# Performance work log

Hardware: AMD Instinct MI355X
Metric: run time of the kernel (lower is better)

Reference implementation:

```python
import jax, jax.numpy as jnp
import numpy as np

C = 0.01          # Poincare ball curvature 1/100
SQRT_C = 0.1
EPS = 1e-15
BALL_EPS = 4e-3   # geoopt float32 projx boundary epsilon


def _norm(x):
    return jnp.linalg.norm(x, axis=-1, keepdims=True)


def expmap0(u):
    n = jnp.maximum(_norm(u), EPS)
    return jnp.tanh(SQRT_C * n) * u / (SQRT_C * n)


def logmap0(x):
    n = jnp.maximum(_norm(x), EPS)
    t = jnp.clip(SQRT_C * n, -1.0 + 1e-7, 1.0 - 1e-7)
    return jnp.arctanh(t) * x / (SQRT_C * n)


def projx(x):
    maxnorm = (1.0 - BALL_EPS) / SQRT_C
    n = jnp.maximum(_norm(x), EPS)
    return jnp.where(n > maxnorm, x / n * maxnorm, x)


def mobius_matvec(M, x):
    xn = jnp.maximum(_norm(x), EPS)
    mx = x @ M.T
    mxn = jnp.maximum(_norm(mx), EPS)
    t = jnp.clip(SQRT_C * xn, -1.0 + 1e-7, 1.0 - 1e-7)
    res = jnp.tanh(mxn / xn * jnp.arctanh(t)) * mx / (mxn * SQRT_C)
    return jnp.where(jnp.all(mx == 0, axis=-1, keepdims=True), 0.0, res)


def mobius_add(x, y):
    x2 = jnp.sum(x * x, -1, keepdims=True)
    y2 = jnp.sum(y * y, -1, keepdims=True)
    xy = jnp.sum(x * y, -1, keepdims=True)
    num = (1 + 2 * C * xy + C * y2) * x + (1 - C * x2) * y
    den = 1 + 2 * C * xy + C * C * x2 * y2
    return num / jnp.maximum(den, EPS)


def hyp_linear(x, W, b):
    # eval mode: weight dropout is a no-op
    res = projx(mobius_matvec(W, x))
    hb = projx(expmap0(b.reshape(1, -1)))
    return projx(mobius_add(res, hb))


def setup_inputs() -> dict:
    key = jax.random.key(0)
    ks = jax.random.split(key, 10)
    B, S, N, H, HEADS, E = 2, 4, 10000, 64, 4, 160000
    G = B * S
    OC = H // HEADS
    # edges guaranteed to have no self-loops (module removes then re-adds them)
    src = jax.random.randint(ks[0], (G, E), 0, N)
    off = jax.random.randint(ks[1], (G, E), 1, N)
    dst = (src + off) % N
    edge_index = jnp.stack([src, dst], axis=1).astype(jnp.int32)  # [G,2,E]

    def glorot(k, shape, fan):
        a = np.sqrt(6.0 / fan)
        return jax.random.uniform(k, shape, minval=-a, maxval=a, dtype=jnp.float32)

    emb = jax.random.normal(ks[2], (N, H), dtype=jnp.float32)
    att_i = glorot(ks[3], (1, HEADS, OC), HEADS * OC + 1)
    att_j = glorot(ks[4], (1, HEADS, OC), HEADS * OC + 1)
    w1 = glorot(ks[5], (H, OC), H + OC)   # HypLinear(in=16, out=64): weight [out,in]
    b1 = jnp.zeros((H,), jnp.float32)
    w2 = glorot(ks[6], (H, H), H + H)
    b2 = jnp.zeros((H,), jnp.float32)
    history_graphs = jnp.zeros((B, S, N), jnp.float32)  # only shape is used
    return {"history_graphs": history_graphs, "edge_index": edge_index,
            "emb": emb, "att_i": att_i, "att_j": att_j,
            "w1": w1, "b1": b1, "w2": w2, "b2": b2}


def reference(history_graphs, edge_index, emb, att_i, att_j, w1, b1, w2, b2):
    B, S, N = history_graphs.shape
    G = edge_index.shape[0]
    H = emb.shape[1]
    heads = att_i.shape[1]
    oc = H // heads

    # node ids are arange(N) for every (b,s) -> identical features per graph
    x0 = projx(expmap0(emb))   # initHyperX, [N,H]
    xt = logmap0(x0)           # tangent features used by attention, [N,H]

    # add self loops (inputs contain none)
    loops = jnp.broadcast_to(jnp.arange(N, dtype=edge_index.dtype)[None, None, :], (G, 2, N))
    ei = jnp.concatenate([edge_index, loops], axis=-1)  # [G,2,E+N]

    def agg(e):
        src, dst = e[0], e[1]                       # targets (i), sources (j)
        x_i = xt[src].reshape(-1, heads, oc)        # [E2,h,oc]
        x_j = xt[dst].reshape(-1, heads, oc)
        alpha = jnp.sum(x_i * att_i, -1) + jnp.sum(x_j * att_j, -1)  # [E2,h]
        alpha = jax.nn.leaky_relu(alpha, 0.2)
        m = jax.ops.segment_max(alpha, src, num_segments=N)
        a = jnp.exp(alpha - m[src])
        s = jax.ops.segment_sum(a, src, num_segments=N)
        a = a / (s[src] + 1e-16)                    # edge softmax; dropout eval no-op
        sup = jax.ops.segment_sum(x_j * a[..., None], src, num_segments=N)  # [N,h,oc]
        sup = sup.mean(axis=1)                      # concat=False -> head mean, [N,oc]
        return projx(expmap0(sup))

    h = jax.vmap(agg)(ei)                           # [G,N,oc]
    node_emb = h.reshape(B, S, N, oc)[:, -1]        # last timestep, [B,N,oc]

    z = hyp_linear(node_emb, w1, b1)                # 16 -> 64
    z = projx(expmap0(jax.nn.silu(logmap0(z))))     # HypAct(SiLU)
    z = projx(expmap0(logmap0(z)))                  # HypDropout (eval: log/exp round trip)
    z = hyp_linear(z, w2, b2)                       # 64 -> 64
    return z
```

## Files before the change

### kernel.cpp

```cpp
#include <hip/hip_runtime.h>
#include <hip/hip_bf16.h>

#define N_NODES 10000
#define NE 160000
#define CAP 96
#define SQRT_C 0.1f
#define CC 0.01f
#define EPS 1e-15f
#define MAXNORM ((1.0f - 4e-3f) / SQRT_C)

__device__ __forceinline__ float ldf(const void* p, int i, int isbf) {
    return isbf ? __bfloat162float(((const __hip_bfloat16*)p)[i])
                : ((const float*)p)[i];
}

__device__ __forceinline__ int sniff_wave(const void* emb, int tid) {
    unsigned wv = ((const unsigned*)emb)[tid & 63];
    unsigned ex = (wv >> 7) & 0xFFu;
    unsigned long long m = __ballot(ex >= 116u && ex <= 133u);
    return (__popcll(m) >= 32) ? 1 : 0;
}

__device__ __forceinline__ float wsum(float v) {
#pragma unroll
    for (int off = 32; off > 0; off >>= 1) v += __shfl_xor(v, off, 64);
    return v;
}
__device__ __forceinline__ float wmax(float v) {
#pragma unroll
    for (int off = 32; off > 0; off >>= 1) v = fmaxf(v, __shfl_xor(v, off, 64));
    return v;
}

#define EDGE_PREAMBLE(T)                                                  \
    int slot = ((T) >= NE) ? 1 : 0;                                       \
    int e = (T) - slot * NE;                                              \
    int g = slot ? 7 : 3;

__global__ __launch_bounds__(256) void pre_scatter(const void* __restrict__ emb,
                                                   const void* __restrict__ att_i,
                                                   const void* __restrict__ att_j,
                                                   const void* __restrict__ w1g,
                                                   const void* __restrict__ b1g,
                                                   const void* __restrict__ w2g,
                                                   const void* __restrict__ b2g,
                                                   const int* __restrict__ ei,
                                                   float* __restrict__ xt,
                                                   float* __restrict__ ai,
                                                   float* __restrict__ aj,
                                                   int* __restrict__ cnt,
                                                   unsigned short* __restrict__ bucket,
                                                   int* __restrict__ ovf_cnt,
                                                   unsigned* __restrict__ ovf,
                                                   int* __restrict__ flag,
                                                   float* __restrict__ wf1t,
                                                   float* __restrict__ wf2t,
                                                   float* __restrict__ hb1f,
                                                   float* __restrict__ hb2f,
                                                   float* __restrict__ hbn2) {
    __shared__ int sflag;
    int tid = threadIdx.x;
    int w = tid >> 6, lane = tid & 63;
    if (blockIdx.x < 2500) {
        if (tid < 64) { int s = sniff_wave(emb, tid); if (tid == 0) sflag = s; }
        __syncthreads();
        int isbf = sflag;
        int t = blockIdx.x * 256 + tid;
        int node = t >> 6;
        float u = ldf(emb, node * 64 + lane, isbf);
        float n = fmaxf(sqrtf(wsum(u * u)), EPS);
        float th = tanhf(SQRT_C * n);
        float x0 = th / (SQRT_C * n) * u;
        float x0n = th / SQRT_C;
        if (x0n > MAXNORM) { x0 *= MAXNORM / x0n; x0n = MAXNORM; }
        float tc = fminf(SQRT_C * x0n, 1.0f - 1e-7f);
        float xv = atanhf(tc) / (SQRT_C * x0n) * x0;
        xt[node * 64 + lane] = xv;
        float pi = xv * ldf(att_i, lane, isbf);
        float pj = xv * ldf(att_j, lane, isbf);
#pragma unroll
        for (int off = 8; off > 0; off >>= 1) {
            pi += __shfl_xor(pi, off, 64);
            pj += __shfl_xor(pj, off, 64);
        }
        if ((lane & 15) == 0) {
            ai[node * 4 + (lane >> 4)] = pi;
            aj[node * 4 + (lane >> 4)] = pj;
        }
    } else if (blockIdx.x < 3750) {
        int t = (blockIdx.x - 2500) * 256 + tid;
        EDGE_PREAMBLE(t);
        int src = ei[g * 2 * NE + e];
        int dst = ei[g * 2 * NE + NE + e];
        int i = slot * N_NODES + src;
        int pos = atomicAdd(&cnt[i], 1);
        if (pos < CAP) bucket[i * CAP + pos] = (unsigned short)dst;
        else {
            int oi = atomicAdd(ovf_cnt, 1);
            ovf[oi] = ((unsigned)slot << 28) | ((unsigned)src << 14) | (unsigned)dst;
        }
    } else {
        if (tid < 64) { int s = sniff_wave(emb, tid); if (tid == 0) sflag = s; }
        __syncthreads();
        int isbf = sflag;
        if (tid == 0) *flag = isbf;
        for (int i = tid; i < 1024; i += 256) {
            int o = i >> 4, c = i & 15;
            wf1t[c * 64 + o] = ldf(w1g, i, isbf);
        }
        for (int i = tid; i < 4096; i += 256) {
            int o = i >> 6, c = i & 63;
            wf2t[c * 64 + o] = ldf(w2g, i, isbf);
        }
        if (w < 2) {
            const void* bg = w ? b2g : b1g;
            float b = ldf(bg, lane, isbf);
            float n = fmaxf(sqrtf(wsum(b * b)), EPS);
            float th = tanhf(SQRT_C * n);
            float hv = th / (SQRT_C * n) * b;
            float hn = th / SQRT_C;
            if (hn > MAXNORM) { hv *= MAXNORM / hn; hn = MAXNORM; }
            (w ? hb2f : hb1f)[lane] = hv;
            if (lane == 0) hbn2[w] = hn * hn;
        }
    }
}

__global__ __launch_bounds__(256) void node_agg(const int* __restrict__ cnt,
                                                const unsigned short* __restrict__ bucket,
                                                const int* __restrict__ ovf_cnt,
                                                const unsigned* __restrict__ ovf,
                                                const float* __restrict__ ai,
                                                const float* __restrict__ aj,
                                                const float* __restrict__ xt,
                                                float* __restrict__ sup_t) {
    __shared__ float wlds[4][64 * 4];
    __shared__ int dlds[4][64];
    int w = threadIdx.x >> 6, lane = threadIdx.x & 63;
    int idx = blockIdx.x * 4 + w;
    int slot = (idx >= N_NODES) ? 1 : 0;
    int n = idx - slot * N_NODES;
    int deg = cnt[idx];
    int start = idx * CAP;

    float4 ai4 = *(const float4*)&ai[n * 4];
    float4 aj4n = *(const float4*)&aj[n * 4];
    float ain[4] = {ai4.x, ai4.y, ai4.z, ai4.w};
    float ajn[4] = {aj4n.x, aj4n.y, aj4n.z, aj4n.w};
    int hh = lane >> 4;
    float acc;

    if (deg <= 63) {
        bool act = (lane <= deg);
        int d = (lane < deg) ? (int)bucket[start + lane] : n;
        float4 a4 = act ? *(const float4*)&aj[d * 4] : make_float4(0.f, 0.f, 0.f, 0.f);
        float ajv[4] = {a4.x, a4.y, a4.z, a4.w};
        float eh[4];
#pragma unroll
        for (int h = 0; h < 4; ++h) {
            float a = ain[h] + ajv[h];
            a = (a < 0.0f) ? 0.2f * a : a;
            eh[h] = act ? expf(a) : 0.0f;
        }
        float sh[4];
#pragma unroll
        for (int h = 0; h < 4; ++h) sh[h] = wsum(eh[h]);
#pragma unroll
        for (int h = 0; h < 4; ++h)
            wlds[w][lane * 4 + h] = eh[h] * (0.25f / (sh[h] + 1e-16f));
        dlds[w][lane] = d;
        int m = deg + 1;
        float a0 = 0.f, a1 = 0.f, a2 = 0.f, a3 = 0.f;
        int e = 0;
        for (; e + 4 <= m; e += 4) {
            int d0 = dlds[w][e], d1 = dlds[w][e + 1];
            int d2 = dlds[w][e + 2], d3 = dlds[w][e + 3];
            float w0 = wlds[w][(e + 0) * 4 + hh], w1 = wlds[w][(e + 1) * 4 + hh];
            float w2 = wlds[w][(e + 2) * 4 + hh], w3 = wlds[w][(e + 3) * 4 + hh];
            a0 = fmaf(w0, xt[d0 * 64 + lane], a0);
            a1 = fmaf(w1, xt[d1 * 64 + lane], a1);
            a2 = fmaf(w2, xt[d2 * 64 + lane], a2);
            a3 = fmaf(w3, xt[d3 * 64 + lane], a3);
        }
        for (; e < m; ++e)
            a0 = fmaf(wlds[w][e * 4 + hh], xt[dlds[w][e] * 64 + lane], a0);
        acc = (a0 + a1) + (a2 + a3);
    } else {
        int bdeg = (deg < CAP) ? deg : CAP;
        int tov = (deg > CAP) ? *ovf_cnt : 0;
        float mh[4];
#pragma unroll
        for (int h = 0; h < 4; ++h) {
            float a = ain[h] + ajn[h];
            mh[h] = (a < 0.0f) ? 0.2f * a : a;
        }
        for (int e = lane; e < bdeg; e += 64) {
            int d = bucket[start + e];
#pragma unroll
            for (int h = 0; h < 4; ++h) {
                float a = ain[h] + aj[d * 4 + h];
                a = (a < 0.0f) ? 0.2f * a : a;
                mh[h] = fmaxf(mh[h], a);
            }
        }
        for (int k = lane; k < tov; k += 64) {
            unsigned pe = ovf[k];
            if ((int)(pe >> 28) == slot && (int)((pe >> 14) & 0x3FFFu) == n) {
                int d = pe & 0x3FFFu;
#pragma unroll
                for (int h = 0; h < 4; ++h) {
                    float a = ain[h] + aj[d * 4 + h];
                    a = (a < 0.0f) ? 0.2f * a : a;
                    mh[h] = fmaxf(mh[h], a);
                }
            }
        }
#pragma unroll
        for (int h = 0; h < 4; ++h) mh[h] = wmax(mh[h]);
        float sh[4] = {0.f, 0.f, 0.f, 0.f};
        if (lane == 0) {
#pragma unroll
            for (int h = 0; h < 4; ++h) {
                float a = ain[h] + ajn[h];
                a = (a < 0.0f) ? 0.2f * a : a;
                sh[h] = expf(a - mh[h]);
            }
        }
        for (int e = lane; e < bdeg; e += 64) {
            int d = bucket[start + e];
#pragma unroll
            for (int h = 0; h < 4; ++h) {
                float a = ain[h] + aj[d * 4 + h];
                a = (a < 0.0f) ? 0.2f * a : a;
                sh[h] += expf(a - mh[h]);
            }
        }
        for (int k = lane; k < tov; k += 64) {
            unsigned pe = ovf[k];
            if ((int)(pe >> 28) == slot && (int)((pe >> 14) & 0x3FFFu) == n) {
                int d = pe & 0x3FFFu;
#pragma unroll
                for (int h = 0; h < 4; ++h) {
                    float a = ain[h] + aj[d * 4 + h];
                    a = (a < 0.0f) ? 0.2f * a : a;
                    sh[h] += expf(a - mh[h]);
                }
            }
        }
#pragma unroll
        for (int h = 0; h < 4; ++h) sh[h] = wsum(sh[h]);
        float scale[4];
#pragma unroll
        for (int h = 0; h < 4; ++h) scale[h] = 0.25f / (sh[h] + 1e-16f);
        float aih = ain[hh], mhh = mh[hh], sch = scale[hh];
        float aself = aih + ajn[hh];
        aself = (aself < 0.0f) ? 0.2f * aself : aself;
        acc = expf(aself - mhh) * sch * xt[n * 64 + lane];
        for (int e = 0; e < bdeg; ++e) {
            int d = bucket[start + e];
            float a = aih + aj[d * 4 + hh];
            a = (a < 0.0f) ? 0.2f * a : a;
            acc = fmaf(expf(a - mhh) * sch, xt[d * 64 + lane], acc);
        }
        for (int k = 0; k < tov; ++k) {
            unsigned pe = ovf[k];
            if ((int)(pe >> 28) == slot && (int)((pe >> 14) & 0x3FFFu) == n) {
                int d = pe & 0x3FFFu;
                float a = aih + aj[d * 4 + hh];
                a = (a < 0.0f) ? 0.2f * a : a;
                acc = fmaf(expf(a - mhh) * sch, xt[d * 64 + lane], acc);
            }
        }
    }
    acc += __shfl_xor(acc, 16, 64);
    acc += __shfl_xor(acc, 32, 64);
    if (lane < 16) sup_t[lane * 20000 + idx] = acc;
}

__global__ __launch_bounds__(256) void final_stage(const float* __restrict__ sup_t,
                                                   const float* __restrict__ wf1t,
                                                   const float* __restrict__ wf2t,
                                                   const float* __restrict__ hb1f,
                                                   const float* __restrict__ hb2f,
                                                   const float* __restrict__ hbn2,
                                                   const int* __restrict__ flag,
                                                   void* __restrict__ outv) {
    __shared__ float Z[65 * 64];
    __shared__ float pA[2][4][64];
    __shared__ float pB[2][4][64];
    int w = threadIdx.x >> 6, lane = threadIdx.x & 63;
    int base = blockIdx.x * 64;
    int nd = base + lane;
    bool valid = (nd < 2 * N_NODES);
    int isbf = *flag;
    float y2a = hbn2[0], y2b = hbn2[1];
    int ob = w * 16;

    float v[16];
#pragma unroll
    for (int c = 0; c < 16; ++c) v[c] = valid ? sup_t[c * 20000 + nd] : 0.0f;
    float n2 = 0.f;
#pragma unroll
    for (int c = 0; c < 16; ++c) n2 = fmaf(v[c], v[c], n2);
    float n = fmaxf(sqrtf(n2), EPS);
    float th0 = tanhf(SQRT_C * n);
    float s0 = th0 / (SQRT_C * n);
    float x0n = th0 / SQRT_C;
    if (x0n > MAXNORM) { s0 *= MAXNORM / x0n; x0n = MAXNORM; }
#pragma unroll
    for (int c = 0; c < 16; ++c) v[c] *= s0;

    float a1[16];
#pragma unroll
    for (int oj = 0; oj < 16; ++oj) a1[oj] = 0.f;
#pragma unroll
    for (int c = 0; c < 16; ++c) {
        float vc = v[c];
#pragma unroll
        for (int oj = 0; oj < 16; ++oj)
            a1[oj] = fmaf(wf1t[c * 64 + ob + oj], vc, a1[oj]);
    }
    float pn = 0.f, ph = 0.f;
#pragma unroll
    for (int oj = 0; oj < 16; ++oj) {
        pn = fmaf(a1[oj], a1[oj], pn);
        ph = fmaf(a1[oj], hb1f[ob + oj], ph);
    }
    pA[0][w][lane] = pn; pA[1][w][lane] = ph;
    __syncthreads();
    float mxn2 = pA[0][0][lane] + pA[0][1][lane] + pA[0][2][lane] + pA[0][3][lane];
    float mxhb = pA[1][0][lane] + pA[1][1][lane] + pA[1][2][lane] + pA[1][3][lane];

    float z2n;
    {
        float xn = fmaxf(x0n, EPS);
        float mxn = fmaxf(sqrtf(mxn2), EPS);
        float t = fminf(SQRT_C * xn, 1.0f - 1e-7f);
        float th = tanhf(mxn / xn * atanhf(t));
        float rs = th / (mxn * SQRT_C);
        float rn = th / SQRT_C;
        if (mxn2 == 0.0f) { rs = 0.f; rn = 0.f; }
        if (rn > MAXNORM) { rs *= MAXNORM / rn; rn = MAXNORM; }
        float xy = rs * mxhb;
        float x2 = rn * rn;
        float A = 1.0f + 2.0f * CC * xy + CC * y2a;
        float B = 1.0f - CC * x2;
        float rden = 1.0f / fmaxf(1.0f + 2.0f * CC * xy + CC * CC * x2 * y2a, EPS);
        float pz = 0.f;
#pragma unroll
        for (int oj = 0; oj < 16; ++oj) {
            float z = (A * rs * a1[oj] + B * hb1f[ob + oj]) * rden;
            a1[oj] = z;
            pz = fmaf(z, z, pz);
        }
        pB[0][w][lane] = pz;
        __syncthreads();
        float zn2 = pB[0][0][lane] + pB[0][1][lane] + pB[0][2][lane] + pB[0][3][lane];
        float zn = fmaxf(sqrtf(zn2), EPS);
        float sc = (zn > MAXNORM) ? MAXNORM / zn : 1.0f;
        float z1n = fminf(zn, MAXNORM);
        float lg = atanhf(fminf(SQRT_C * z1n, 1.0f - 1e-7f)) / (SQRT_C * z1n) * sc;
        float pu = 0.f;
#pragma unroll
        for (int oj = 0; oj < 16; ++oj) {
            float u = lg * a1[oj];
            u = u / (1.0f + expf(-u));
            a1[oj] = u;
            pu = fmaf(u, u, pu);
        }
        pA[0][w][lane] = pu;
        __syncthreads();
        float un2 = pA[0][0][lane] + pA[0][1][lane] + pA[0][2][lane] + pA[0][3][lane];
        float un = fmaxf(sqrtf(un2), EPS);
        float th2 = tanhf(SQRT_C * un);
        float s2 = th2 / (SQRT_C * un);
        z2n = th2 / SQRT_C;
        if (z2n > MAXNORM) { s2 *= MAXNORM / z2n; z2n = MAXNORM; }
#pragma unroll
        for (int oj = 0; oj < 16; ++oj) Z[(ob + oj) * 64 + lane] = a1[oj] * s2;
    }
    __syncthreads();

    float a2[16];
#pragma unroll
    for (int oj = 0; oj < 16; ++oj) a2[oj] = 0.f;
#pragma unroll 4
    for (int c = 0; c < 64; ++c) {
        float zc = Z[c * 64 + lane];
#pragma unroll
        for (int oj = 0; oj < 16; ++oj)
            a2[oj] = fmaf(wf2t[c * 64 + ob + oj], zc, a2[oj]);
    }
    float pn2 = 0.f, ph2 = 0.f;
#pragma unroll
    for (int oj = 0; oj < 16; ++oj) {
        pn2 = fmaf(a2[oj], a2[oj], pn2);
        ph2 = fmaf(a2[oj], hb2f[ob + oj], ph2);
    }
    pB[0][w][lane] = pn2; pB[1][w][lane] = ph2;
    __syncthreads();
    float mxn2b = pB[0][0][lane] + pB[0][1][lane] + pB[0][2][lane] + pB[0][3][lane];
    float mxhb2 = pB[1][0][lane] + pB[1][1][lane] + pB[1][2][lane] + pB[1][3][lane];
    {
        float xn = fmaxf(z2n, EPS);
        float mxn = fmaxf(sqrtf(mxn2b), EPS);
        float t = fminf(SQRT_C * xn, 1.0f - 1e-7f);
        float th = tanhf(mxn / xn * atanhf(t));
        float rs = th / (mxn * SQRT_C);
        float rn = th / SQRT_C;
        if (mxn2b == 0.0f) { rs = 0.f; rn = 0.f; }
        if (rn > MAXNORM) { rs *= MAXNORM / rn; rn = MAXNORM; }
        float xy = rs * mxhb2;
        float x2 = rn * rn;
        float A = 1.0f + 2.0f * CC * xy + CC * y2b;
        float B = 1.0f - CC * x2;
        float rden = 1.0f / fmaxf(1.0f + 2.0f * CC * xy + CC * CC * x2 * y2b, EPS);
        float pz = 0.f;
#pragma unroll
        for (int oj = 0; oj < 16; ++oj) {
            float z = (A * rs * a2[oj] + B * hb2f[ob + oj]) * rden;
            a2[oj] = z;
            pz = fmaf(z, z, pz);
        }
        pA[0][w][lane] = pz;
        __syncthreads();
        float zn2 = pA[0][0][lane] + pA[0][1][lane] + pA[0][2][lane] + pA[0][3][lane];
        float zn = fmaxf(sqrtf(zn2), EPS);
        float s4 = (zn > MAXNORM) ? MAXNORM / zn : 1.0f;
#pragma unroll
        for (int oj = 0; oj < 16; ++oj) Z[(ob + oj) * 65 + lane] = a2[oj] * s4;
    }
    __syncthreads();

#pragma unroll 1
    for (int k = 0; k < 16; ++k) {
        int nl = w * 16 + k;
        int ng = base + nl;
        if (ng >= 2 * N_NODES) break;
        float val = Z[lane * 65 + nl];
        if (isbf) ((__hip_bfloat16*)outv)[ng * 64 + lane] = __float2bfloat16(val);
        else      ((float*)outv)[ng * 64 + lane] = val;
    }
}

extern "C" void kernel_launch(void* const* d_in, const int* in_sizes, int n_in,
                              void* d_out, int out_size, void* d_ws, size_t ws_size,
                              hipStream_t stream) {
    const int* ei = (const int*)d_in[1];
    const void* emb   = d_in[2];
    const void* att_i = d_in[3];
    const void* att_j = d_in[4];
    const void* w1 = d_in[5];
    const void* b1 = d_in[6];
    const void* w2 = d_in[7];
    const void* b2 = d_in[8];

    float* ws = (float*)d_ws;
    float* xt    = ws;
    float* ai    = ws + 640000;
    float* aj    = ws + 680000;
    float* sup_t = ws + 720000;
    int* cnt     = (int*)(ws + 1040000);
    int* ovf_cnt = (int*)(ws + 1060000);
    unsigned short* bucket = (unsigned short*)(ws + 1060032);
    unsigned* ovf = (unsigned*)(ws + 2020032);
    int* flag     = (int*)(ws + 2340032);
    float* wf1t = ws + 2340064;
    float* wf2t = ws + 2341088;
    float* hb1f = ws + 2345184;
    float* hb2f = ws + 2345248;
    float* hbn2 = ws + 2345312;

    hipMemsetAsync((void*)cnt, 0, (2 * N_NODES + 8) * sizeof(int), stream);
    hipLaunchKernelGGL(pre_scatter, dim3(3751), dim3(256), 0, stream,
                       emb, att_i, att_j, w1, b1, w2, b2, ei,
                       xt, ai, aj, cnt, bucket, ovf_cnt, ovf, flag,
                       wf1t, wf2t, hb1f, hb2f, hbn2);
    hipLaunchKernelGGL(node_agg, dim3(5000), dim3(256), 0, stream,
                       cnt, bucket, ovf_cnt, ovf, ai, aj, xt, sup_t);
    hipLaunchKernelGGL(final_stage, dim3(313), dim3(256), 0, stream,
                       sup_t, wf1t, wf2t, hb1f, hb2f, hbn2, flag, d_out);
}
```

Baseline: 151.8 us.

## Fuse node aggregation and final hyperbolic MLP stage into one kernel

Merges the node_agg and final_stage kernels into a single 1024-thread kernel. Each block aggregates 64 nodes (16 waves handling 4 nodes each) into shared memory, then 4 waves run the two hyperbolic linear layers on those nodes. This drops the global sup_t round trip and one kernel launch. In exchange the grid shrinks to 313 blocks with launch bounds of one block per CU, which reduces parallelism and latency hiding for the gather-heavy aggregation, and 12 waves sit idle during the final stage.

```diff
diff --git a/kernel.cpp b/kernel.cpp
--- a/kernel.cpp
+++ b/kernel.cpp
@@ -126,87 +126,91 @@
     }
 }
 
-__global__ __launch_bounds__(256) void node_agg(const int* __restrict__ cnt,
-                                                const unsigned short* __restrict__ bucket,
-                                                const int* __restrict__ ovf_cnt,
-                                                const unsigned* __restrict__ ovf,
-                                                const float* __restrict__ ai,
-                                                const float* __restrict__ aj,
-                                                const float* __restrict__ xt,
-                                                float* __restrict__ sup_t) {
-    __shared__ float wlds[4][64 * 4];
-    __shared__ int dlds[4][64];
-    int w = threadIdx.x >> 6, lane = threadIdx.x & 63;
-    int idx = blockIdx.x * 4 + w;
-    int slot = (idx >= N_NODES) ? 1 : 0;
-    int n = idx - slot * N_NODES;
-    int deg = cnt[idx];
-    int start = idx * CAP;
-
-    float4 ai4 = *(const float4*)&ai[n * 4];
-    float4 aj4n = *(const float4*)&aj[n * 4];
-    float ain[4] = {ai4.x, ai4.y, ai4.z, ai4.w};
-    float ajn[4] = {aj4n.x, aj4n.y, aj4n.z, aj4n.w};
+__global__ __launch_bounds__(1024, 1) void agg_final(const int* __restrict__ cnt,
+                                                     const unsigned short* __restrict__ bucket,
+                                                     const int* __restrict__ ovf_cnt,
+                                                     const unsigned* __restrict__ ovf,
+                                                     const float* __restrict__ ai,
+                                                     const float* __restrict__ aj,
+                                                     const float* __restrict__ xt,
+                                                     const float* __restrict__ wf1t,
+                                                     const float* __restrict__ wf2t,
+                                                     const float* __restrict__ hb1f,
+                                                     const float* __restrict__ hb2f,
+                                                     const float* __restrict__ hbn2,
+                                                     const int* __restrict__ flag,
+                                                     void* __restrict__ outv) {
+    __shared__ float arena[5184];
+    __shared__ float sups[64 * 17];
+    int tid = threadIdx.x;
+    int w16 = tid >> 6, lane = tid & 63;
+    int base = blockIdx.x * 64;
+
+    float* wlds = &arena[w16 * 256];
+    int* dlds = (int*)&arena[4096] + w16 * 64;
     int hh = lane >> 4;
-    float acc;
-
-    if (deg <= 63) {
-        bool act = (lane <= deg);
-        int d = (lane < deg) ? (int)bucket[start + lane] : n;
-        float4 a4 = act ? *(const float4*)&aj[d * 4] : make_float4(0.f, 0.f, 0.f, 0.f);
-        float ajv[4] = {a4.x, a4.y, a4.z, a4.w};
-        float eh[4];
-#pragma unroll
-        for (int h = 0; h < 4; ++h) {
-            float a = ain[h] + ajv[h];
-            a = (a < 0.0f) ? 0.2f * a : a;
-            eh[h] = act ? expf(a) : 0.0f;
-        }
-        float sh[4];
-#pragma unroll
-        for (int h = 0; h < 4; ++h) sh[h] = wsum(eh[h]);
-#pragma unroll
-        for (int h = 0; h < 4; ++h)
-            wlds[w][lane * 4 + h] = eh[h] * (0.25f / (sh[h] + 1e-16f));
-        dlds[w][lane] = d;
-        int m = deg + 1;
-        float a0 = 0.f, a1 = 0.f, a2 = 0.f, a3 = 0.f;
-        int e = 0;
-        for (; e + 4 <= m; e += 4) {
-            int d0 = dlds[w][e], d1 = dlds[w][e + 1];
-            int d2 = dlds[w][e + 2], d3 = dlds[w][e + 3];
-            float w0 = wlds[w][(e + 0) * 4 + hh], w1 = wlds[w][(e + 1) * 4 + hh];
-            float w2 = wlds[w][(e + 2) * 4 + hh], w3 = wlds[w][(e + 3) * 4 + hh];
-            a0 = fmaf(w0, xt[d0 * 64 + lane], a0);
-            a1 = fmaf(w1, xt[d1 * 64 + lane], a1);
-            a2 = fmaf(w2, xt[d2 * 64 + lane], a2);
-            a3 = fmaf(w3, xt[d3 * 64 + lane], a3);
-        }
-        for (; e < m; ++e)
-            a0 = fmaf(wlds[w][e * 4 + hh], xt[dlds[w][e] * 64 + lane], a0);
-        acc = (a0 + a1) + (a2 + a3);
-    } else {
-        int bdeg = (deg < CAP) ? deg : CAP;
-        int tov = (deg > CAP) ? *ovf_cnt : 0;
-        float mh[4];
-#pragma unroll
-        for (int h = 0; h < 4; ++h) {
-            float a = ain[h] + ajn[h];
-            mh[h] = (a < 0.0f) ? 0.2f * a : a;
-        }
-        for (int e = lane; e < bdeg; e += 64) {
-            int d = bucket[start + e];
+#pragma unroll 1
+    for (int r = 0; r < 4; ++r) {
+        int nl = w16 * 4 + r;
+        int idx = base + nl;
+        if (idx >= 2 * N_NODES) break;
+        int slot = (idx >= N_NODES) ? 1 : 0;
+        int n = idx - slot * N_NODES;
+        int deg = cnt[idx];
+        int start = idx * CAP;
+
+        float4 ai4 = *(const float4*)&ai[n * 4];
+        float4 aj4n = *(const float4*)&aj[n * 4];
+        float ain[4] = {ai4.x, ai4.y, ai4.z, ai4.w};
+        float ajn[4] = {aj4n.x, aj4n.y, aj4n.z, aj4n.w};
+        float acc;
+
+        if (deg <= 63) {
+            bool act = (lane <= deg);
+            int d = (lane < deg) ? (int)bucket[start + lane] : n;
+            float4 a4 = act ? *(const float4*)&aj[d * 4] : make_float4(0.f, 0.f, 0.f, 0.f);
+            float ajv[4] = {a4.x, a4.y, a4.z, a4.w};
+            float eh[4];
 #pragma unroll
             for (int h = 0; h < 4; ++h) {
-                float a = ain[h] + aj[d * 4 + h];
+                float a = ain[h] + ajv[h];
                 a = (a < 0.0f) ? 0.2f * a : a;
-                mh[h] = fmaxf(mh[h], a);
-            }
-        }
-        for (int k = lane; k < tov; k += 64) {
-            unsigned pe = ovf[k];
-            if ((int)(pe >> 28) == slot && (int)((pe >> 14) & 0x3FFFu) == n) {
-                int d = pe & 0x3FFFu;
+                eh[h] = act ? expf(a) : 0.0f;
+            }
+            float sh[4];
+#pragma unroll
+            for (int h = 0; h < 4; ++h) sh[h] = wsum(eh[h]);
+#pragma unroll
+            for (int h = 0; h < 4; ++h)
+                wlds[lane * 4 + h] = eh[h] * (0.25f / (sh[h] + 1e-16f));
+            dlds[lane] = d;
+            int m = deg + 1;
+            float a0 = 0.f, a1 = 0.f, a2 = 0.f, a3 = 0.f;
+            int e = 0;
+            for (; e + 4 <= m; e += 4) {
+                int d0 = dlds[e], d1 = dlds[e + 1];
+                int d2 = dlds[e + 2], d3 = dlds[e + 3];
+                float w0 = wlds[(e + 0) * 4 + hh], w1 = wlds[(e + 1) * 4 + hh];
+                float w2 = wlds[(e + 2) * 4 + hh], w3 = wlds[(e + 3) * 4 + hh];
+                a0 = fmaf(w0, xt[d0 * 64 + lane], a0);
+                a1 = fmaf(w1, xt[d1 * 64 + lane], a1);
+                a2 = fmaf(w2, xt[d2 * 64 + lane], a2);
+                a3 = fmaf(w3, xt[d3 * 64 + lane], a3);
+            }
+            for (; e < m; ++e)
+                a0 = fmaf(wlds[e * 4 + hh], xt[dlds[e] * 64 + lane], a0);
+            acc = (a0 + a1) + (a2 + a3);
+        } else {
+            int bdeg = (deg < CAP) ? deg : CAP;
+            int tov = (deg > CAP) ? *ovf_cnt : 0;
+            float mh[4];
+#pragma unroll
+            for (int h = 0; h < 4; ++h) {
+                float a = ain[h] + ajn[h];
+                mh[h] = (a < 0.0f) ? 0.2f * a : a;
+            }
+            for (int e = lane; e < bdeg; e += 64) {
+                int d = bucket[start + e];
 #pragma unroll
                 for (int h = 0; h < 4; ++h) {
                     float a = ain[h] + aj[d * 4 + h];
@@ -214,31 +218,31 @@
                     mh[h] = fmaxf(mh[h], a);
                 }
             }
-        }
-#pragma unroll
-        for (int h = 0; h < 4; ++h) mh[h] = wmax(mh[h]);
-        float sh[4] = {0.f, 0.f, 0.f, 0.f};
-        if (lane == 0) {
-#pragma unroll
-            for (int h = 0; h < 4; ++h) {
-                float a = ain[h] + ajn[h];
-                a = (a < 0.0f) ? 0.2f * a : a;
-                sh[h] = expf(a - mh[h]);
-            }
-        }
-        for (int e = lane; e < bdeg; e += 64) {
-            int d = bucket[start + e];
-#pragma unroll
-            for (int h = 0; h < 4; ++h) {
-                float a = ain[h] + aj[d * 4 + h];
-                a = (a < 0.0f) ? 0.2f * a : a;
-                sh[h] += expf(a - mh[h]);
-            }
-        }
-        for (int k = lane; k < tov; k += 64) {
-            unsigned pe = ovf[k];
-            if ((int)(pe >> 28) == slot && (int)((pe >> 14) & 0x3FFFu) == n) {
-                int d = pe & 0x3FFFu;
+            for (int k = lane; k < tov; k += 64) {
+                unsigned pe = ovf[k];
+                if ((int)(pe >> 28) == slot && (int)((pe >> 14) & 0x3FFFu) == n) {
+                    int d = pe & 0x3FFFu;
+#pragma unroll
+                    for (int h = 0; h < 4; ++h) {
+                        float a = ain[h] + aj[d * 4 + h];
+                        a = (a < 0.0f) ? 0.2f * a : a;
+                        mh[h] = fmaxf(mh[h], a);
+                    }
+                }
+            }
+#pragma unroll
+            for (int h = 0; h < 4; ++h) mh[h] = wmax(mh[h]);
+            float sh[4] = {0.f, 0.f, 0.f, 0.f};
+            if (lane == 0) {
+#pragma unroll
+                for (int h = 0; h < 4; ++h) {
+                    float a = ain[h] + ajn[h];
+                    a = (a < 0.0f) ? 0.2f * a : a;
+                    sh[h] = expf(a - mh[h]);
+                }
+            }
+            for (int e = lane; e < bdeg; e += 64) {
+                int d = bucket[start + e];
 #pragma unroll
                 for (int h = 0; h < 4; ++h) {
                     float a = ain[h] + aj[d * 4 + h];
@@ -246,50 +250,54 @@
                     sh[h] += expf(a - mh[h]);
                 }
             }
-        }
-#pragma unroll
-        for (int h = 0; h < 4; ++h) sh[h] = wsum(sh[h]);
-        float scale[4];
-#pragma unroll
-        for (int h = 0; h < 4; ++h) scale[h] = 0.25f / (sh[h] + 1e-16f);
-        float aih = ain[hh], mhh = mh[hh], sch = scale[hh];
-        float aself = aih + ajn[hh];
-        aself = (aself < 0.0f) ? 0.2f * aself : aself;
-        acc = expf(aself - mhh) * sch * xt[n * 64 + lane];
-        for (int e = 0; e < bdeg; ++e) {
-            int d = bucket[start + e];
-            float a = aih + aj[d * 4 + hh];
-            a = (a < 0.0f) ? 0.2f * a : a;
-            acc = fmaf(expf(a - mhh) * sch, xt[d * 64 + lane], acc);
-        }
-        for (int k = 0; k < tov; ++k) {
-            unsigned pe = ovf[k];
-            if ((int)(pe >> 28) == slot && (int)((pe >> 14) & 0x3FFFu) == n) {
-                int d = pe & 0x3FFFu;
+            for (int k = lane; k < tov; k += 64) {
+                unsigned pe = ovf[k];
+                if ((int)(pe >> 28) == slot && (int)((pe >> 14) & 0x3FFFu) == n) {
+                    int d = pe & 0x3FFFu;
+#pragma unroll
+                    for (int h = 0; h < 4; ++h) {
+                        float a = ain[h] + aj[d * 4 + h];
+                        a = (a < 0.0f) ? 0.2f * a : a;
+                        sh[h] += expf(a - mh[h]);
+                    }
+                }
+            }
+#pragma unroll
+            for (int h = 0; h < 4; ++h) sh[h] = wsum(sh[h]);
+            float scale[4];
+#pragma unroll
+            for (int h = 0; h < 4; ++h) scale[h] = 0.25f / (sh[h] + 1e-16f);
+            float aih = ain[hh], mhh = mh[hh], sch = scale[hh];
+            float aself = aih + ajn[hh];
+            aself = (aself < 0.0f) ? 0.2f * aself : aself;
+            acc = expf(aself - mhh) * sch * xt[n * 64 + lane];
+            for (int e = 0; e < bdeg; ++e) {
+                int d = bucket[start + e];
                 float a = aih + aj[d * 4 + hh];
                 a = (a < 0.0f) ? 0.2f * a : a;
                 acc = fmaf(expf(a - mhh) * sch, xt[d * 64 + lane], acc);
             }
-        }
-    }
-    acc += __shfl_xor(acc, 16, 64);
-    acc += __shfl_xor(acc, 32, 64);
-    if (lane < 16) sup_t[lane * 20000 + idx] = acc;
-}
-
-__global__ __launch_bounds__(256) void final_stage(const float* __restrict__ sup_t,
-                                                   const float* __restrict__ wf1t,
-                                                   const float* __restrict__ wf2t,
-                                                   const float* __restrict__ hb1f,
-                                                   const float* __restrict__ hb2f,
-                                                   const float* __restrict__ hbn2,
-                                                   const int* __restrict__ flag,
-                                                   void* __restrict__ outv) {
-    __shared__ float Z[65 * 64];
-    __shared__ float pA[2][4][64];
-    __shared__ float pB[2][4][64];
-    int w = threadIdx.x >> 6, lane = threadIdx.x & 63;
-    int base = blockIdx.x * 64;
+            for (int k = 0; k < tov; ++k) {
+                unsigned pe = ovf[k];
+                if ((int)(pe >> 28) == slot && (int)((pe >> 14) & 0x3FFFu) == n) {
+                    int d = pe & 0x3FFFu;
+                    float a = aih + aj[d * 4 + hh];
+                    a = (a < 0.0f) ? 0.2f * a : a;
+                    acc = fmaf(expf(a - mhh) * sch, xt[d * 64 + lane], acc);
+                }
+            }
+        }
+        acc += __shfl_xor(acc, 16, 64);
+        acc += __shfl_xor(acc, 32, 64);
+        if (lane < 16) sups[nl * 17 + lane] = acc;
+    }
+    __syncthreads();
+    if (w16 >= 4) return;
+
+    float* Z = arena;
+    float* pA = &arena[4160];
+    float* pB = &arena[4672];
+    int w = w16;
     int nd = base + lane;
     bool valid = (nd < 2 * N_NODES);
     int isbf = *flag;
@@ -298,7 +306,7 @@
 
     float v[16];
 #pragma unroll
-    for (int c = 0; c < 16; ++c) v[c] = valid ? sup_t[c * 20000 + nd] : 0.0f;
+    for (int c = 0; c < 16; ++c) v[c] = valid ? sups[lane * 17 + c] : 0.0f;
     float n2 = 0.f;
 #pragma unroll
     for (int c = 0; c < 16; ++c) n2 = fmaf(v[c], v[c], n2);
@@ -326,10 +334,12 @@
         pn = fmaf(a1[oj], a1[oj], pn);
         ph = fmaf(a1[oj], hb1f[ob + oj], ph);
     }
-    pA[0][w][lane] = pn; pA[1][w][lane] = ph;
+    pA[0 * 256 + w * 64 + lane] = pn; pA[1 * 256 + w * 64 + lane] = ph;
     __syncthreads();
-    float mxn2 = pA[0][0][lane] + pA[0][1][lane] + pA[0][2][lane] + pA[0][3][lane];
-    float mxhb = pA[1][0][lane] + pA[1][1][lane] + pA[1][2][lane] + pA[1][3][lane];
+    float mxn2 = pA[0 * 256 + lane] + pA[0 * 256 + 64 + lane] +
+                 pA[0 * 256 + 128 + lane] + pA[0 * 256 + 192 + lane];
+    float mxhb = pA[1 * 256 + lane] + pA[1 * 256 + 64 + lane] +
+                 pA[1 * 256 + 128 + lane] + pA[1 * 256 + 192 + lane];
 
     float z2n;
     {
@@ -353,9 +363,9 @@
             a1[oj] = z;
             pz = fmaf(z, z, pz);
         }
-        pB[0][w][lane] = pz;
+        pB[w * 64 + lane] = pz;
         __syncthreads();
-        float zn2 = pB[0][0][lane] + pB[0][1][lane] + pB[0][2][lane] + pB[0][3][lane];
+        float zn2 = pB[lane] + pB[64 + lane] + pB[128 + lane] + pB[192 + lane];
         float zn = fmaxf(sqrtf(zn2), EPS);
         float sc = (zn > MAXNORM) ? MAXNORM / zn : 1.0f;
         float z1n = fminf(zn, MAXNORM);
@@ -368,9 +378,9 @@
             a1[oj] = u;
             pu = fmaf(u, u, pu);
         }
-        pA[0][w][lane] = pu;
+        pA[w * 64 + lane] = pu;
         __syncthreads();
-        float un2 = pA[0][0][lane] + pA[0][1][lane] + pA[0][2][lane] + pA[0][3][lane];
+        float un2 = pA[lane] + pA[64 + lane] + pA[128 + lane] + pA[192 + lane];
         float un = fmaxf(sqrtf(un2), EPS);
         float th2 = tanhf(SQRT_C * un);
         float s2 = th2 / (SQRT_C * un);
@@ -397,10 +407,12 @@
         pn2 = fmaf(a2[oj], a2[oj], pn2);
         ph2 = fmaf(a2[oj], hb2f[ob + oj], ph2);
     }
-    pB[0][w][lane] = pn2; pB[1][w][lane] = ph2;
+    pB[0 * 256 + w * 64 + lane] = pn2; pB[1 * 256 + w * 64 + lane] = ph2;
     __syncthreads();
-    float mxn2b = pB[0][0][lane] + pB[0][1][lane] + pB[0][2][lane] + pB[0][3][lane];
-    float mxhb2 = pB[1][0][lane] + pB[1][1][lane] + pB[1][2][lane] + pB[1][3][lane];
+    float mxn2b = pB[0 * 256 + lane] + pB[0 * 256 + 64 + lane] +
+                  pB[0 * 256 + 128 + lane] + pB[0 * 256 + 192 + lane];
+    float mxhb2 = pB[1 * 256 + lane] + pB[1 * 256 + 64 + lane] +
+                  pB[1 * 256 + 128 + lane] + pB[1 * 256 + 192 + lane];
     {
         float xn = fmaxf(z2n, EPS);
         float mxn = fmaxf(sqrtf(mxn2b), EPS);
@@ -422,9 +434,9 @@
             a2[oj] = z;
             pz = fmaf(z, z, pz);
         }
-        pA[0][w][lane] = pz;
+        pA[w * 64 + lane] = pz;
         __syncthreads();
-        float zn2 = pA[0][0][lane] + pA[0][1][lane] + pA[0][2][lane] + pA[0][3][lane];
+        float zn2 = pA[lane] + pA[64 + lane] + pA[128 + lane] + pA[192 + lane];
         float zn = fmaxf(sqrtf(zn2), EPS);
         float s4 = (zn > MAXNORM) ? MAXNORM / zn : 1.0f;
 #pragma unroll
@@ -459,7 +471,6 @@
     float* xt    = ws;
     float* ai    = ws + 640000;
     float* aj    = ws + 680000;
-    float* sup_t = ws + 720000;
     int* cnt     = (int*)(ws + 1040000);
     int* ovf_cnt = (int*)(ws + 1060000);
     unsigned short* bucket = (unsigned short*)(ws + 1060032);
@@ -476,8 +487,7 @@
                        emb, att_i, att_j, w1, b1, w2, b2, ei,
                        xt, ai, aj, cnt, bucket, ovf_cnt, ovf, flag,
                        wf1t, wf2t, hb1f, hb2f, hbn2);
-    hipLaunchKernelGGL(node_agg, dim3(5000), dim3(256), 0, stream,
-                       cnt, bucket, ovf_cnt, ovf, ai, aj, xt, sup_t);
-    hipLaunchKernelGGL(final_stage, dim3(313), dim3(256), 0, stream,
-                       sup_t, wf1t, wf2t, hb1f, hb2f, hbn2, flag, d_out);
-}
+    hipLaunchKernelGGL(agg_final, dim3(313), dim3(1024), 0, stream,
+                       cnt, bucket, ovf_cnt, ovf, ai, aj, xt,
+                       wf1t, wf2t, hb1f, hb2f, hbn2, flag, d_out);
+}
```

After: 161.3 us. +6.3%, slower.
